# Performance work log

Measured on AMD Instinct MI355X. Metric: run time of the kernel, lower is better.

## Reference

```python
import jax, jax.numpy as jnp
import numpy as np

N_NODES = 50000
N_EDGES = 800000
NODE_DIM = 128
EDGE_DIM = 16
OUT_DIM = 64
HEADS = 4


def setup_inputs() -> dict:
    key = jax.random.key(0)
    ks = jax.random.split(key, 12)
    x = jax.random.normal(ks[0], (N_NODES, NODE_DIM), jnp.float32)
    edge_index = jax.random.randint(ks[1], (2, N_EDGES), 0, N_NODES)
    batch = jnp.zeros((N_NODES,), jnp.int32)
    edge_attr = jax.random.normal(ks[2], (N_EDGES, EDGE_DIM), jnp.float32)
    s = 1.0 / np.sqrt(NODE_DIM)
    W = jax.random.normal(ks[3], (NODE_DIM, HEADS * OUT_DIM), jnp.float32) * s
    att_src = jax.random.normal(ks[4], (HEADS, OUT_DIM), jnp.float32) * 0.1
    att_dst = jax.random.normal(ks[5], (HEADS, OUT_DIM), jnp.float32) * 0.1
    W_e = jax.random.normal(ks[6], (EDGE_DIM, HEADS * OUT_DIM), jnp.float32) * (1.0 / np.sqrt(EDGE_DIM))
    att_edge = jax.random.normal(ks[7], (HEADS, OUT_DIM), jnp.float32) * 0.1
    bias = jnp.zeros((OUT_DIM,), jnp.float32)
    gamma = jnp.ones((OUT_DIM,), jnp.float32)
    beta = jnp.zeros((OUT_DIM,), jnp.float32)
    return {"x": x, "edge_index": edge_index, "batch": batch, "edge_attr": edge_attr,
            "W": W, "att_src": att_src, "att_dst": att_dst, "W_e": W_e,
            "att_edge": att_edge, "bias": bias, "gamma": gamma, "beta": beta}


def reference(x, edge_index, batch, edge_attr, W, att_src, att_dst, W_e, att_edge, bias, gamma, beta):
    N = x.shape[0]
    H, C = att_src.shape
    src, dst = edge_index[0], edge_index[1]
    E = src.shape[0]

    # add self loops; self-loop edge_attr = per-node mean of incoming edge attrs (PyG fill_value='mean')
    cnt = jax.ops.segment_sum(jnp.ones((E, 1), x.dtype), dst, num_segments=N)
    loop_attr = jax.ops.segment_sum(edge_attr, dst, num_segments=N) / jnp.maximum(cnt, 1.0)
    loop_idx = jnp.arange(N, dtype=src.dtype)
    src_f = jnp.concatenate([src, loop_idx])
    dst_f = jnp.concatenate([dst, loop_idx])
    ea = jnp.concatenate([edge_attr, loop_attr], axis=0)

    h = (x @ W).reshape(N, H, C)                       # [N,H,C]
    a_src = jnp.einsum('nhc,hc->nh', h, att_src)       # [N,H]
    a_dst = jnp.einsum('nhc,hc->nh', h, att_dst)
    e_emb = (ea @ W_e).reshape(-1, H, C)               # [E',H,C]
    a_edge = jnp.einsum('ehc,hc->eh', e_emb, att_edge)

    alpha = jax.nn.leaky_relu(a_src[src_f] + a_dst[dst_f] + a_edge, 0.2)  # [E',H]
    amax = jax.ops.segment_max(alpha, dst_f, num_segments=N)
    expa = jnp.exp(alpha - amax[dst_f])
    denom = jax.ops.segment_sum(expa, dst_f, num_segments=N)
    att = expa / (denom[dst_f] + 1e-16)                # segment softmax over dst

    msg = h[src_f] * att[:, :, None]                   # [E',H,C]
    out = jax.ops.segment_sum(msg, dst_f, num_segments=N)  # [N,H,C]
    out = out.mean(axis=1) + bias                      # concat=False -> head mean

    mu = out.mean(-1, keepdims=True)
    var = out.var(-1, keepdims=True)
    out = (out - mu) / jnp.sqrt(var + 1e-5) * gamma + beta
    return jax.nn.elu(out)
```

## Files before the change

kernel.cpp:

```cpp
#include <hip/hip_runtime.h>

typedef unsigned int u32;
typedef unsigned short u16;

static constexpr int NN  = 50000;
static constexpr int EE  = 800000;
static constexpr int CAP = 64;

typedef __attribute__((ext_vector_type(8))) short bf16x8;
typedef __attribute__((ext_vector_type(4))) float f32x4;
typedef __attribute__((ext_vector_type(4))) u32   u32x4;

__device__ inline float u2f(u32 u){ union{u32 i; float f;} v; v.i=u; return v.f; }
__device__ inline float bf2f(u16 u){ return u2f(((u32)u)<<16); }
__device__ inline u16 f2bf(float f){ union{float f; u32 i;} v; v.f=f; u32 i=v.i;
    return (u16)((i + 0x7fffu + ((i>>16)&1u))>>16); }
__device__ inline u32 pk2(float a, float b){ return (u32)f2bf(a) | ((u32)f2bf(b)<<16); }
__device__ inline float lrelu(float x){ return x > 0.f ? x : 0.2f*x; }

__device__ inline u32 pkh(float a, float b){
    union{ _Float16 h[2]; u32 u; } v;
    v.h[0] = (_Float16)a; v.h[1] = (_Float16)b;
    return v.u;
}
__device__ inline float hlo(u32 u){ union{u32 u; _Float16 h[2];} v; v.u=u; return (float)v.h[0]; }
__device__ inline float hhi(u32 u){ union{u32 u; _Float16 h[2];} v; v.u=u; return (float)v.h[1]; }

__device__ inline float ld(const void* base, size_t i, int f32m){
    return f32m ? ((const float*)base)[i] : bf2f(((const u16*)base)[i]);
}

__device__ inline float wsum(float v){
    #pragma unroll
    for (int m=1;m<64;m<<=1) v += __shfl_xor(v, m, 64);
    return v;
}

#if defined(__has_builtin)
#if __has_builtin(__builtin_amdgcn_fdot2_f32_bf16)
#define HAS_DOT2 1
#endif
#endif

#ifdef HAS_DOT2
typedef __attribute__((ext_vector_type(2))) __bf16 bf16x2;
#endif

__device__ inline float dot2acc(u32 hv, u32 wv, float acc){
#ifdef HAS_DOT2
    union { u32 u; bf16x2 v; } a, b; a.u = hv; b.u = wv;
    return __builtin_amdgcn_fdot2_f32_bf16(a.v, b.v, acc, false);
#else
    acc = fmaf(u2f(hv<<16),         u2f(wv<<16),         acc);
    acc = fmaf(u2f(hv&0xffff0000u), u2f(wv&0xffff0000u), acc);
    return acc;
#endif
}

__device__ inline int detect_f32(const u16* xraw){
    int lane = threadIdx.x & 63;
    bool bad = false;
    #pragma unroll
    for (int i = 0; i < 8; ++i){
        float v = bf2f(xraw[2*(lane + i*64)]);
        if (!(fabsf(v) < 1e10f)) bad = true;
    }
    return __any(bad) ? 1 : 0;
}

__device__ inline void edge_logits(const void* ea, int e, int f32m,
                                   const float* Ml, float* A){
    float v[16];
    if (f32m){
        const f32x4* r = ((const f32x4*)ea) + (size_t)e*4;
        f32x4 a = __builtin_nontemporal_load(r);
        f32x4 b = __builtin_nontemporal_load(r+1);
        f32x4 c = __builtin_nontemporal_load(r+2);
        f32x4 d = __builtin_nontemporal_load(r+3);
        v[0]=a[0]; v[1]=a[1]; v[2]=a[2]; v[3]=a[3];
        v[4]=b[0]; v[5]=b[1]; v[6]=b[2]; v[7]=b[3];
        v[8]=c[0]; v[9]=c[1]; v[10]=c[2]; v[11]=c[3];
        v[12]=d[0]; v[13]=d[1]; v[14]=d[2]; v[15]=d[3];
    } else {
        const u32x4* r = ((const u32x4*)ea) + (size_t)e*2;
        u32x4 q0 = __builtin_nontemporal_load(r);
        u32x4 q1 = __builtin_nontemporal_load(r+1);
        v[0]=u2f(q0[0]<<16); v[1]=u2f(q0[0]&0xffff0000u);
        v[2]=u2f(q0[1]<<16); v[3]=u2f(q0[1]&0xffff0000u);
        v[4]=u2f(q0[2]<<16); v[5]=u2f(q0[2]&0xffff0000u);
        v[6]=u2f(q0[3]<<16); v[7]=u2f(q0[3]&0xffff0000u);
        v[8]=u2f(q1[0]<<16); v[9]=u2f(q1[0]&0xffff0000u);
        v[10]=u2f(q1[1]<<16); v[11]=u2f(q1[1]&0xffff0000u);
        v[12]=u2f(q1[2]<<16); v[13]=u2f(q1[2]&0xffff0000u);
        v[14]=u2f(q1[3]<<16); v[15]=u2f(q1[3]&0xffff0000u);
    }
    float a0=0,a1=0,a2=0,a3=0;
    #pragma unroll
    for (int j = 0; j < 16; ++j){
        a0 = fmaf(v[j], Ml[j*4+0], a0);
        a1 = fmaf(v[j], Ml[j*4+1], a1);
        a2 = fmaf(v[j], Ml[j*4+2], a2);
        a3 = fmaf(v[j], Ml[j*4+3], a3);
    }
    A[0]=a0; A[1]=a1; A[2]=a2; A[3]=a3;
}

__global__ __launch_bounds__(256) void k_prep(const u16* __restrict__ xraw,
                                              const void* __restrict__ W,
                                              const void* __restrict__ att_src,
                                              const void* __restrict__ att_dst,
                                              const void* __restrict__ W_e,
                                              const void* __restrict__ att_edge,
                                              int* __restrict__ flag,
                                              u16* __restrict__ Wt,
                                              float* __restrict__ Mv){
    int f32m = detect_f32(xraw);
    int b = blockIdx.x, t = threadIdx.x;
    if (b == 0){
        if (t == 0) *flag = f32m;
        if (t < 64){
            int d = t >> 2, h = t & 3;
            float s = 0.f;
            for (int c = 0; c < 64; ++c)
                s += ld(W_e, d*256 + h*64 + c, f32m) * ld(att_edge, h*64 + c, f32m);
            Mv[t] = s;
        }
    } else if (b <= 128){
        int i = (b-1)*256 + t;
        int k = i >> 8, n = i & 255;
        Wt[n*128 + k] = f2bf(ld(W, (size_t)k*256 + n, f32m));
    } else {
        int i = (b-129)*256 + t;
        int c = i >> 7, k = i & 127;
        float s = 0.f;
        if (c < 8){
            int h = c & 3;
            const void* att = (c < 4) ? att_src : att_dst;
            for (int j = 0; j < 64; ++j)
                s += ld(W, (size_t)k*256 + h*64 + j, f32m) * ld(att, h*64 + j, f32m);
        }
        Wt[(size_t)(256 + c)*128 + k] = f2bf(s);
    }
}

static constexpr int LDSROW = 136;
static constexpr int CROW   = 264;

__global__ __launch_bounds__(256) void k_gx(const void* __restrict__ x,
                                            const u16* __restrict__ Wt,
                                            const int* __restrict__ flag,
                                            u16* __restrict__ hbuf,
                                            float* __restrict__ a_src,
                                            float* __restrict__ a_dst,
                                            const int* __restrict__ ei,
                                            const void* __restrict__ ea,
                                            const float* __restrict__ Mv,
                                            int* __restrict__ deg,
                                            u32* __restrict__ brec,
                                            int N, int E, int GB){
    __shared__ u16 sh[64*CROW];
    int t = threadIdx.x;
    int f32m = *flag;
    if ((int)blockIdx.x < GB){
        int row0 = blockIdx.x*64;
        if (f32m){
            const f32x4* xg = (const f32x4*)x;
            #pragma unroll
            for (int j=0;j<8;++j){
                int idx = t + j*256;
                int r = idx >> 5, c4 = idx & 31;
                int gr = row0 + r; if (gr >= N) gr = N-1;
                f32x4 v = __builtin_nontemporal_load(&xg[(size_t)gr*32 + c4]);
                *(uint2*)&sh[r*LDSROW + c4*4] = make_uint2(pk2(v[0],v[1]), pk2(v[2],v[3]));
            }
        } else {
            const u32x4* xg = (const u32x4*)x;
            #pragma unroll
            for (int j=0;j<4;++j){
                int idx = t + j*256;
                int r = idx >> 4, c8 = idx & 15;
                int gr = row0 + r; if (gr >= N) gr = N-1;
                u32x4 v = __builtin_nontemporal_load(&xg[(size_t)gr*16 + c8]);
                *(u32x4*)&sh[r*LDSROW + c8*8] = v;
            }
        }
        __syncthreads();
        int wave = t >> 6, lane = t & 63;
        int l15 = lane & 15, quad = lane >> 4;
        int mrow = wave*16 + l15;
        bf16x8 afr[4];
        #pragma unroll
        for (int s=0;s<4;++s)
            afr[s] = *(const bf16x8*)&sh[mrow*LDSROW + s*32 + quad*8];
        __syncthreads();
        f32x4 acc[17];
        #pragma unroll
        for (int tl=0;tl<17;++tl){
            f32x4 a = {0.f,0.f,0.f,0.f};
            #pragma unroll
            for (int s=0;s<4;++s){
                bf16x8 bfr = *(const bf16x8*)&Wt[(size_t)(tl*16 + l15)*128 + s*32 + quad*8];
                a = __builtin_amdgcn_mfma_f32_16x16x32_bf16(afr[s], bfr, a, 0, 0, 0);
            }
            acc[tl] = a;
        }
        int rbase = row0 + wave*16 + quad*4;
        #pragma unroll
        for (int r=0;r<4;++r){
            int gr = rbase + r;
            if (gr < N){
                if (l15 < 4)      a_src[gr*4 + l15]     = acc[16][r];
                else if (l15 < 8) a_dst[gr*4 + (l15-4)] = acc[16][r];
            }
        }
        #pragma unroll
        for (int r=0;r<4;++r){
            int row = wave*16 + quad*4 + r;
            #pragma unroll
            for (int tl=0;tl<4;++tl){
                u32 lo = pk2(acc[tl  ][r], acc[tl+4 ][r]);
                u32 hi = pk2(acc[tl+8][r], acc[tl+12][r]);
                *(uint2*)&sh[row*CROW + (tl*16 + l15)*4] = make_uint2(lo, hi);
            }
        }
        __syncthreads();
        uint4* h4 = (uint4*)hbuf;
        #pragma unroll
        for (int j=0;j<8;++j){
            int idx = t + j*256;
            int row = idx >> 5, c16 = idx & 31;
            if (row0 + row < N){
                uint4 v = *(const uint4*)&sh[row*CROW + c16*8];
                h4[(size_t)(row0 + row)*32 + c16] = v;
            }
        }
    } else {
        float* Ml = (float*)sh;
        if (t < 64) Ml[t] = Mv[t];
        __syncthreads();
        int base = ((int)blockIdx.x - GB)*512 + t;
        #pragma unroll
        for (int j=0;j<2;++j){
            int e = base + j*256;
            if (e >= E) continue;
            int src = __builtin_nontemporal_load(&ei[e]);
            int dst = __builtin_nontemporal_load(&ei[E + e]);
            float A[4];
            edge_logits(ea, e, f32m, Ml, A);
            int slot = atomicAdd(&deg[dst], 1);
            if (slot < CAP){
                size_t i3 = ((size_t)dst*CAP + slot)*3;
                brec[i3]   = (u32)src;
                brec[i3+1] = pkh(A[0], A[1]);
                brec[i3+2] = pkh(A[2], A[3]);
            }
        }
    }
}

__global__ __launch_bounds__(256) void k_node(const int* __restrict__ deg,
                                              const u32* __restrict__ brec,
                                              const float* __restrict__ a_src,
                                              const float* __restrict__ a_dst,
                                              const u16* __restrict__ hbuf,
                                              const void* __restrict__ bias,
                                              const void* __restrict__ gamma,
                                              const void* __restrict__ beta,
                                              const int* __restrict__ flag,
                                              void* __restrict__ out, int N){
    __shared__ uint4 lrec[4][CAP+4];
    int f32m = *flag;
    int lane = threadIdx.x & 63;
    int slot = threadIdx.x >> 6;
    int n = blockIdx.x*4 + slot;
    int dg = deg[n];
    int dc = dg < CAP ? dg : CAP;
    float4 an  = ((const float4*)a_src)[n];
    float4 adn = ((const float4*)a_dst)[n];
    bool v0 = lane < dc;
    u32 src = (u32)n;
    float w0=0.f,w1=0.f,w2=0.f,w3=0.f;
    float a0=0.f,a1=0.f,a2=0.f,a3=0.f;
    if (v0){
        const u32* rp = brec + ((size_t)n*CAP + lane)*3;
        u32 s   = __builtin_nontemporal_load(&rp[0]);
        u32 p01 = __builtin_nontemporal_load(&rp[1]);
        u32 p23 = __builtin_nontemporal_load(&rp[2]);
        src = s;
        a0 = hlo(p01); a1 = hhi(p01); a2 = hlo(p23); a3 = hhi(p23);
        float4 asg = ((const float4*)a_src)[s];
        w0 = expf(lrelu(asg.x + adn.x + a0));
        w1 = expf(lrelu(asg.y + adn.y + a1));
        w2 = expf(lrelu(asg.z + adn.z + a2));
        w3 = expf(lrelu(asg.w + adn.w + a3));
    }
    float dn0 = wsum(w0), dn1 = wsum(w1), dn2 = wsum(w2), dn3 = wsum(w3);
    float invd = 1.f / (float)(dg > 1 ? dg : 1);
    float ge0 = wsum(a0)*invd, ge1 = wsum(a1)*invd;
    float ge2 = wsum(a2)*invd, ge3 = wsum(a3)*invd;
    float exS0 = expf(lrelu(an.x + adn.x + ge0));
    float exS1 = expf(lrelu(an.y + adn.y + ge1));
    float exS2 = expf(lrelu(an.z + adn.z + ge2));
    float exS3 = expf(lrelu(an.w + adn.w + ge3));
    float i0 = 0.25f/(dn0 + exS0 + 1e-16f);
    float i1 = 0.25f/(dn1 + exS1 + 1e-16f);
    float i2 = 0.25f/(dn2 + exS2 + 1e-16f);
    float i3 = 0.25f/(dn3 + exS3 + 1e-16f);
    if (v0)
        lrec[slot][lane] = make_uint4(src, pk2(w0*i0, w1*i1), pk2(w2*i2, w3*i3), 0u);
    if (lane == 0)
        lrec[slot][dc] = make_uint4((u32)n, pk2(exS0*i0, exS1*i1), pk2(exS2*i2, exS3*i3), 0u);
    else if (lane <= 3)
        lrec[slot][dc + lane] = make_uint4((u32)n, 0u, 0u, 0u);
    __syncthreads();
    int T = dc + 1;
    int iters = (T + 3) >> 2;
    int half = lane >> 5, l5 = lane & 31;
    const uint4* hb4 = (const uint4*)hbuf;
    float acc0 = 0.f, acc1 = 0.f;
    uint4 rA0 = lrec[slot][half];
    uint4 rA1 = lrec[slot][2 + half];
    uint4 hA0 = hb4[(size_t)rA0.x*32 + l5];
    uint4 hA1 = hb4[(size_t)rA1.x*32 + l5];
    uint4 rB0, rB1, hB0, hB1;
    if (iters > 1){
        rB0 = lrec[slot][4 + half];
        rB1 = lrec[slot][6 + half];
        hB0 = hb4[(size_t)rB0.x*32 + l5];
        hB1 = hb4[(size_t)rB1.x*32 + l5];
    }
    int i = 0;
    while (true){
        {
            bool pf = (i + 2 < iters);
            uint4 nr0, nr1, nh0, nh1;
            if (pf){
                nr0 = lrec[slot][4*(i+2) + half];
                nr1 = lrec[slot][4*(i+2) + 2 + half];
                nh0 = hb4[(size_t)nr0.x*32 + l5];
                nh1 = hb4[(size_t)nr1.x*32 + l5];
            }
            acc0 = dot2acc(hA0.x, rA0.y, acc0);
            acc0 = dot2acc(hA0.y, rA0.z, acc0);
            acc1 = dot2acc(hA0.z, rA0.y, acc1);
            acc1 = dot2acc(hA0.w, rA0.z, acc1);
            acc0 = dot2acc(hA1.x, rA1.y, acc0);
            acc0 = dot2acc(hA1.y, rA1.z, acc0);
            acc1 = dot2acc(hA1.z, rA1.y, acc1);
            acc1 = dot2acc(hA1.w, rA1.z, acc1);
            if (pf){ rA0=nr0; rA1=nr1; hA0=nh0; hA1=nh1; }
            if (++i >= iters) break;
        }
        {
            bool pf = (i + 2 < iters);
            uint4 nr0, nr1, nh0, nh1;
            if (pf){
                nr0 = lrec[slot][4*(i+2) + half];
                nr1 = lrec[slot][4*(i+2) + 2 + half];
                nh0 = hb4[(size_t)nr0.x*32 + l5];
                nh1 = hb4[(size_t)nr1.x*32 + l5];
            }
            acc0 = dot2acc(hB0.x, rB0.y, acc0);
            acc0 = dot2acc(hB0.y, rB0.z, acc0);
            acc1 = dot2acc(hB0.z, rB0.y, acc1);
            acc1 = dot2acc(hB0.w, rB0.z, acc1);
            acc0 = dot2acc(hB1.x, rB1.y, acc0);
            acc0 = dot2acc(hB1.y, rB1.z, acc0);
            acc1 = dot2acc(hB1.z, rB1.y, acc1);
            acc1 = dot2acc(hB1.w, rB1.z, acc1);
            if (pf){ rB0=nr0; rB1=nr1; hB0=nh0; hB1=nh1; }
            if (++i >= iters) break;
        }
    }
    acc0 += __shfl_xor(acc0, 32, 64);
    acc1 += __shfl_xor(acc1, 32, 64);
    float va = __shfl(acc0, lane>>1, 64);
    float vb = __shfl(acc1, lane>>1, 64);
    float o = ((lane & 1) ? vb : va) + ld(bias, lane, f32m);
    float mu = wsum(o) * (1.f/64.f);
    float d = o - mu;
    float var = wsum(d*d) * (1.f/64.f);
    float y = d * rsqrtf(var + 1e-5f) * ld(gamma, lane, f32m) + ld(beta, lane, f32m);
    y = y > 0.f ? y : expf(y) - 1.f;
    if (f32m) __builtin_nontemporal_store(y, &((float*)out)[(size_t)n*64 + lane]);
    else      __builtin_nontemporal_store(f2bf(y), &((u16*)out)[(size_t)n*64 + lane]);
}

extern "C" void kernel_launch(void* const* d_in, const int* in_sizes, int n_in,
                              void* d_out, int out_size, void* d_ws, size_t ws_size,
                              hipStream_t stream){
    const void* x        = d_in[0];
    const int*  ei       = (const int*)d_in[1];
    const void* ea       = d_in[3];
    const void* W        = d_in[4];
    const void* att_src  = d_in[5];
    const void* att_dst  = d_in[6];
    const void* W_e      = d_in[7];
    const void* att_edge = d_in[8];
    const void* bias     = d_in[9];
    const void* gamma    = d_in[10];
    const void* beta     = d_in[11];
    const int N = NN, E = EE;

    char* p = (char*)d_ws;
    auto alloc = [&](size_t bytes){ void* r = (void*)p; p += (bytes + 255) & ~(size_t)255; return r; };
    int*   deg   = (int*)  alloc((size_t)N*4);
    float* Mv    = (float*)alloc(64*4);
    float* a_src = (float*)alloc((size_t)N*16);
    float* a_dst = (float*)alloc((size_t)N*16);
    u32*   brec  = (u32*)  alloc((size_t)N*CAP*12);
    u16*   hbuf  = (u16*)  alloc((size_t)N*256*2);
    u16*   Wt    = (u16*)  alloc((size_t)272*128*2);
    int*   flag  = (int*)  alloc(256);

    const int GB = (N + 63)/64;
    const int EB = (E + 511)/512;

    hipMemsetAsync(deg, 0, (size_t)N*4, stream);
    k_prep<<<137, 256, 0, stream>>>((const u16*)x, W, att_src, att_dst, W_e, att_edge,
                                    flag, Wt, Mv);
    k_gx<<<GB + EB, 256, 0, stream>>>(x, Wt, flag, hbuf, a_src, a_dst,
                                      ei, ea, Mv, deg, brec, N, E, GB);
    k_node<<<N/4, 256, 0, stream>>>(deg, brec, a_src, a_dst, hbuf,
                                    bias, gamma, beta, flag, d_out, N);
}
```

Baseline: 277.5 us.

## Drop LDS staging in GEMM, pad edge records to 16B, fold deg memset into prep

The node GEMM now loads its A fragments straight from global memory instead of staging x through shared memory, and writes h directly from the accumulators. Wt is permuted so each head-interleaved column layout comes out right without an LDS transpose. Edge records grow from 12 to 16 bytes so each can be written and read as a single uint4. The deg memset is folded into the prep kernel, and the edge blocks handle one edge per thread and read Mv from global memory. The direct h stores are scattered 2-byte writes and the records take more memory, so memory traffic may rise even as syncs and one launch go away.

Result: no change. 275.0 us (-0.9%).

```diff
diff --git a/kernel.cpp b/kernel.cpp
--- a/kernel.cpp
+++ b/kernel.cpp
@@ -69,7 +69,7 @@
 }
 
 __device__ inline void edge_logits(const void* ea, int e, int f32m,
-                                   const float* Ml, float* A){
+                                   const float* __restrict__ Ml, float* A){
     float v[16];
     if (f32m){
         const f32x4* r = ((const f32x4*)ea) + (size_t)e*4;
@@ -113,7 +113,8 @@
                                               const void* __restrict__ att_edge,
                                               int* __restrict__ flag,
                                               u16* __restrict__ Wt,
-                                              float* __restrict__ Mv){
+                                              float* __restrict__ Mv,
+                                              int* __restrict__ deg){
     int f32m = detect_f32(xraw);
     int b = blockIdx.x, t = threadIdx.x;
     if (b == 0){
@@ -127,9 +128,10 @@
         }
     } else if (b <= 128){
         int i = (b-1)*256 + t;
-        int k = i >> 8, n = i & 255;
-        Wt[n*128 + k] = f2bf(ld(W, (size_t)k*256 + n, f32m));
-    } else {
+        int k = i >> 8, j = i & 255;
+        int n = (j & 3)*64 + (j >> 2);
+        Wt[j*128 + k] = f2bf(ld(W, (size_t)k*256 + n, f32m));
+    } else if (b <= 136){
         int i = (b-129)*256 + t;
         int c = i >> 7, k = i & 127;
         float s = 0.f;
@@ -140,11 +142,11 @@
                 s += ld(W, (size_t)k*256 + h*64 + j, f32m) * ld(att, h*64 + j, f32m);
         }
         Wt[(size_t)(256 + c)*128 + k] = f2bf(s);
-    }
-}
-
-static constexpr int LDSROW = 136;
-static constexpr int CROW   = 264;
+    } else {
+        int i = (b-137)*256 + t;
+        if (i < NN) deg[i] = 0;
+    }
+}
 
 __global__ __launch_bounds__(256) void k_gx(const void* __restrict__ x,
                                             const u16* __restrict__ Wt,
@@ -156,43 +158,34 @@
                                             const void* __restrict__ ea,
                                             const float* __restrict__ Mv,
                                             int* __restrict__ deg,
-                                            u32* __restrict__ brec,
+                                            uint4* __restrict__ brec,
                                             int N, int E, int GB){
-    __shared__ u16 sh[64*CROW];
     int t = threadIdx.x;
     int f32m = *flag;
     if ((int)blockIdx.x < GB){
         int row0 = blockIdx.x*64;
-        if (f32m){
-            const f32x4* xg = (const f32x4*)x;
-            #pragma unroll
-            for (int j=0;j<8;++j){
-                int idx = t + j*256;
-                int r = idx >> 5, c4 = idx & 31;
-                int gr = row0 + r; if (gr >= N) gr = N-1;
-                f32x4 v = __builtin_nontemporal_load(&xg[(size_t)gr*32 + c4]);
-                *(uint2*)&sh[r*LDSROW + c4*4] = make_uint2(pk2(v[0],v[1]), pk2(v[2],v[3]));
-            }
-        } else {
-            const u32x4* xg = (const u32x4*)x;
-            #pragma unroll
-            for (int j=0;j<4;++j){
-                int idx = t + j*256;
-                int r = idx >> 4, c8 = idx & 15;
-                int gr = row0 + r; if (gr >= N) gr = N-1;
-                u32x4 v = __builtin_nontemporal_load(&xg[(size_t)gr*16 + c8]);
-                *(u32x4*)&sh[r*LDSROW + c8*8] = v;
-            }
-        }
-        __syncthreads();
         int wave = t >> 6, lane = t & 63;
         int l15 = lane & 15, quad = lane >> 4;
-        int mrow = wave*16 + l15;
+        int grow = row0 + wave*16 + l15; if (grow >= N) grow = N-1;
         bf16x8 afr[4];
-        #pragma unroll
-        for (int s=0;s<4;++s)
-            afr[s] = *(const bf16x8*)&sh[mrow*LDSROW + s*32 + quad*8];
-        __syncthreads();
+        if (f32m){
+            const f32x4* xf = (const f32x4*)x;
+            #pragma unroll
+            for (int s=0;s<4;++s){
+                f32x4 v0 = __builtin_nontemporal_load(&xf[(size_t)grow*32 + s*8 + quad*2]);
+                f32x4 v1 = __builtin_nontemporal_load(&xf[(size_t)grow*32 + s*8 + quad*2 + 1]);
+                union{ u32x4 u; bf16x8 b; } cv;
+                cv.u[0] = pk2(v0[0],v0[1]); cv.u[1] = pk2(v0[2],v0[3]);
+                cv.u[2] = pk2(v1[0],v1[1]); cv.u[3] = pk2(v1[2],v1[3]);
+                afr[s] = cv.b;
+            }
+        } else {
+            const u16* x16 = (const u16*)x;
+            #pragma unroll
+            for (int s=0;s<4;++s)
+                afr[s] = __builtin_nontemporal_load(
+                    (const bf16x8*)&x16[(size_t)grow*128 + s*32 + quad*8]);
+        }
         f32x4 acc[17];
         #pragma unroll
         for (int tl=0;tl<17;++tl){
@@ -215,51 +208,30 @@
         }
         #pragma unroll
         for (int r=0;r<4;++r){
-            int row = wave*16 + quad*4 + r;
-            #pragma unroll
-            for (int tl=0;tl<4;++tl){
-                u32 lo = pk2(acc[tl  ][r], acc[tl+4 ][r]);
-                u32 hi = pk2(acc[tl+8][r], acc[tl+12][r]);
-                *(uint2*)&sh[row*CROW + (tl*16 + l15)*4] = make_uint2(lo, hi);
-            }
-        }
-        __syncthreads();
-        uint4* h4 = (uint4*)hbuf;
-        #pragma unroll
-        for (int j=0;j<8;++j){
-            int idx = t + j*256;
-            int row = idx >> 5, c16 = idx & 31;
-            if (row0 + row < N){
-                uint4 v = *(const uint4*)&sh[row*CROW + c16*8];
-                h4[(size_t)(row0 + row)*32 + c16] = v;
+            int gr = rbase + r;
+            if (gr < N){
+                #pragma unroll
+                for (int tl=0;tl<16;++tl)
+                    hbuf[(size_t)gr*256 + tl*16 + l15] = f2bf(acc[tl][r]);
             }
         }
     } else {
-        float* Ml = (float*)sh;
-        if (t < 64) Ml[t] = Mv[t];
-        __syncthreads();
-        int base = ((int)blockIdx.x - GB)*512 + t;
-        #pragma unroll
-        for (int j=0;j<2;++j){
-            int e = base + j*256;
-            if (e >= E) continue;
+        int e = ((int)blockIdx.x - GB)*256 + t;
+        if (e < E){
             int src = __builtin_nontemporal_load(&ei[e]);
             int dst = __builtin_nontemporal_load(&ei[E + e]);
+            int slot = atomicAdd(&deg[dst], 1);
             float A[4];
-            edge_logits(ea, e, f32m, Ml, A);
-            int slot = atomicAdd(&deg[dst], 1);
-            if (slot < CAP){
-                size_t i3 = ((size_t)dst*CAP + slot)*3;
-                brec[i3]   = (u32)src;
-                brec[i3+1] = pkh(A[0], A[1]);
-                brec[i3+2] = pkh(A[2], A[3]);
-            }
+            edge_logits(ea, e, f32m, Mv, A);
+            if (slot < CAP)
+                brec[(size_t)dst*CAP + slot] =
+                    make_uint4((u32)src, pkh(A[0], A[1]), pkh(A[2], A[3]), 0u);
         }
     }
 }
 
 __global__ __launch_bounds__(256) void k_node(const int* __restrict__ deg,
-                                              const u32* __restrict__ brec,
+                                              const uint4* __restrict__ brec,
                                               const float* __restrict__ a_src,
                                               const float* __restrict__ a_dst,
                                               const u16* __restrict__ hbuf,
@@ -282,13 +254,11 @@
     float w0=0.f,w1=0.f,w2=0.f,w3=0.f;
     float a0=0.f,a1=0.f,a2=0.f,a3=0.f;
     if (v0){
-        const u32* rp = brec + ((size_t)n*CAP + lane)*3;
-        u32 s   = __builtin_nontemporal_load(&rp[0]);
-        u32 p01 = __builtin_nontemporal_load(&rp[1]);
-        u32 p23 = __builtin_nontemporal_load(&rp[2]);
-        src = s;
-        a0 = hlo(p01); a1 = hhi(p01); a2 = hlo(p23); a3 = hhi(p23);
-        float4 asg = ((const float4*)a_src)[s];
+        const u32x4* rp = (const u32x4*)brec + ((size_t)n*CAP + lane);
+        u32x4 r = __builtin_nontemporal_load(rp);
+        src = r[0];
+        a0 = hlo(r[1]); a1 = hhi(r[1]); a2 = hlo(r[2]); a3 = hhi(r[2]);
+        float4 asg = ((const float4*)a_src)[src];
         w0 = expf(lrelu(asg.x + adn.x + a0));
         w1 = expf(lrelu(asg.y + adn.y + a1));
         w2 = expf(lrelu(asg.z + adn.z + a2));
@@ -408,17 +378,17 @@
     float* Mv    = (float*)alloc(64*4);
     float* a_src = (float*)alloc((size_t)N*16);
     float* a_dst = (float*)alloc((size_t)N*16);
-    u32*   brec  = (u32*)  alloc((size_t)N*CAP*12);
+    uint4* brec  = (uint4*)alloc((size_t)N*CAP*16);
     u16*   hbuf  = (u16*)  alloc((size_t)N*256*2);
     u16*   Wt    = (u16*)  alloc((size_t)272*128*2);
     int*   flag  = (int*)  alloc(256);
 
     const int GB = (N + 63)/64;
-    const int EB = (E + 511)/512;
-
-    hipMemsetAsync(deg, 0, (size_t)N*4, stream);
-    k_prep<<<137, 256, 0, stream>>>((const u16*)x, W, att_src, att_dst, W_e, att_edge,
-                                    flag, Wt, Mv);
+    const int EB = (E + 255)/256;
+    const int PB = 137 + (N + 255)/256;
+
+    k_prep<<<PB, 256, 0, stream>>>((const u16*)x, W, att_src, att_dst, W_e, att_edge,
+                                   flag, Wt, Mv, deg);
     k_gx<<<GB + EB, 256, 0, stream>>>(x, Wt, flag, hbuf, a_src, a_dst,
                                       ei, ea, Mv, deg, brec, N, E, GB);
     k_node<<<N/4, 256, 0, stream>>>(deg, brec, a_src, a_dst, hbuf,
```
